# Performance work log

Hardware: AMD Instinct MI355X
Metric: run time of the kernel (lower is better)

The kernel has to match this reference:

```python
import jax, jax.numpy as jnp
import numpy as np

B, NQ, NKV, D = 2, 2048, 4096, 1024
H, DH = 16, 64            # qk_channels = v_channels = 1024 -> 16 heads x 64
HID = 2 * int(4.0 * D)    # GEGLU produces 8192 -> split into 2x4096
EPS = 1e-6


def layernorm(x, scale, bias):
    mu = jnp.mean(x, axis=-1, keepdims=True)
    var = jnp.mean(jnp.square(x - mu), axis=-1, keepdims=True)
    return (x - mu) * jax.lax.rsqrt(var + EPS) * scale + bias


def setup_inputs() -> dict:
    key = jax.random.key(0)
    ks = jax.random.split(key, 12)
    s = 0.02
    return {
        "inputs_q": jax.random.normal(ks[0], (B, NQ, D), jnp.float32),
        "inputs_kv": jax.random.normal(ks[1], (B, NKV, D), jnp.float32),
        "ln_q_scale": jnp.ones((D,), jnp.float32),
        "ln_q_bias": jnp.zeros((D,), jnp.float32),
        "ln_kv_scale": jnp.ones((D,), jnp.float32),
        "ln_kv_bias": jnp.zeros((D,), jnp.float32),
        "Wq": s * jax.random.normal(ks[2], (D, H, DH), jnp.float32),
        "bq": jnp.zeros((H, DH), jnp.float32),
        "Wk": s * jax.random.normal(ks[3], (D, H, DH), jnp.float32),
        "bk": jnp.zeros((H, DH), jnp.float32),
        "Wv": s * jax.random.normal(ks[4], (D, H, DH), jnp.float32),
        "bv": jnp.zeros((H, DH), jnp.float32),
        "Wo": s * jax.random.normal(ks[5], (H, DH, D), jnp.float32),
        "bo": jnp.zeros((D,), jnp.float32),
        "ln2_scale": jnp.ones((D,), jnp.float32),
        "ln2_bias": jnp.zeros((D,), jnp.float32),
        "W1": s * jax.random.normal(ks[6], (D, HID), jnp.float32),
        "b1": jnp.zeros((HID,), jnp.float32),
        "W2": s * jax.random.normal(ks[7], (HID // 2, D), jnp.float32),
        "b2": jnp.zeros((D,), jnp.float32),
    }


def reference(inputs_q, inputs_kv, ln_q_scale, ln_q_bias, ln_kv_scale, ln_kv_bias,
              Wq, bq, Wk, bk, Wv, bv, Wo, bo, ln2_scale, ln2_bias, W1, b1, W2, b2):
    ln_q = layernorm(inputs_q, ln_q_scale, ln_q_bias)
    ln_kv = layernorm(inputs_kv, ln_kv_scale, ln_kv_bias)
    # multi-head projections: DenseGeneral to (H, DH)
    q = jnp.einsum('bqd,dhe->bqhe', ln_q, Wq) + bq
    k = jnp.einsum('bkd,dhe->bkhe', ln_kv, Wk) + bk
    v = jnp.einsum('bkd,dhe->bkhe', ln_kv, Wv) + bv
    # scaled dot-product attention (full score matrix, as in source)
    attn = jnp.einsum('bqhd,bkhd->bhqk', q, k) / np.sqrt(DH).astype(np.float32)
    attn = jax.nn.softmax(attn, axis=-1)
    o = jnp.einsum('bhqk,bkhd->bqhd', attn, v)
    # output projection contracting (H, DH)
    x = jnp.einsum('bqhd,hdo->bqo', o, Wo) + bo
    x = x + inputs_q  # query residual
    # GEGLU MLP
    h = layernorm(x, ln2_scale, ln2_bias)
    h = jnp.dot(h, W1) + b1
    a, g = jnp.split(h, 2, axis=-1)
    h = a * jax.nn.gelu(g)  # approximate (tanh) gelu, flax default
    y = jnp.dot(h, W2) + b2
    return x + y
```

## Files before the change

kernel.cpp:

```cpp
#include <hip/hip_runtime.h>

typedef unsigned short u16;
typedef unsigned int u32;
typedef float f32x4 __attribute__((ext_vector_type(4)));
typedef float f32x16 __attribute__((ext_vector_type(16)));
typedef __bf16 bf16x8 __attribute__((ext_vector_type(8)));
typedef short s16x8 __attribute__((ext_vector_type(8)));
typedef short s16x4 __attribute__((ext_vector_type(4)));
typedef u32 u32x4 __attribute__((ext_vector_type(4)));

#define MFMA16(a, b, c) __builtin_amdgcn_mfma_f32_16x16x32_bf16((a), (b), (c), 0, 0, 0)
#define MFMA32(a, b, c) __builtin_amdgcn_mfma_f32_32x32x16_bf16((a), (b), (c), 0, 0, 0)

typedef const __attribute__((address_space(1))) void* gas1_t;
typedef __attribute__((address_space(3))) void* las3_t;
#define GLDS16(g, l) __builtin_amdgcn_global_load_lds((gas1_t)(g), (las3_t)(l), 16, 0, 0)

static __device__ __forceinline__ u16 f2bf(float f) {
  u32 u = __builtin_bit_cast(u32, f);
  u += 0x7FFFu + ((u >> 16) & 1u);
  return (u16)(u >> 16);
}
static __device__ __forceinline__ float bf2f(u16 h) {
  return __builtin_bit_cast(float, (u32)h << 16);
}
static __device__ __forceinline__ u32 cvtpk(float lo, float hi) {
  u32 r;
  asm("v_cvt_pk_bf16_f32 %0, %1, %2" : "=v"(r) : "v"(lo), "v"(hi));
  return r;
}

__global__ __launch_bounds__(256) void transp_cvt(const float* __restrict__ in,
                                                  u16* __restrict__ out, int K, int N,
                                                  float scale) {
  __shared__ u16 t[64][72];
  int k0 = blockIdx.x * 64, n0 = blockIdx.y * 64;
#pragma unroll
  for (int i = 0; i < 16; ++i) {
    int idx = threadIdx.x + i * 256;
    int r = idx >> 6, c = idx & 63;
    t[r][c] = f2bf(in[(size_t)(k0 + r) * N + n0 + c] * scale);
  }
  __syncthreads();
#pragma unroll
  for (int i = 0; i < 16; ++i) {
    int idx = threadIdx.x + i * 256;
    int r = idx >> 6, c = idx & 63;
    out[(size_t)(n0 + r) * K + k0 + c] = t[c][r];
  }
}

__global__ __launch_bounds__(256) void ln_bf16(const float* __restrict__ x,
                                               const float* __restrict__ sc,
                                               const float* __restrict__ bi,
                                               u16* __restrict__ out) {
  int row = blockIdx.x;
  int tid = threadIdx.x;
  float4 v = ((const float4*)(x + (size_t)row * 1024))[tid];
  float s = v.x + v.y + v.z + v.w;
  float s2 = v.x * v.x + v.y * v.y + v.z * v.z + v.w * v.w;
  for (int m = 1; m < 64; m <<= 1) {
    s += __shfl_xor(s, m);
    s2 += __shfl_xor(s2, m);
  }
  __shared__ float rs[4], rs2[4];
  int wave = tid >> 6, lane = tid & 63;
  if (lane == 0) { rs[wave] = s; rs2[wave] = s2; }
  __syncthreads();
  s = rs[0] + rs[1] + rs[2] + rs[3];
  s2 = rs2[0] + rs2[1] + rs2[2] + rs2[3];
  float mu = s * (1.0f / 1024.0f);
  float var = s2 * (1.0f / 1024.0f) - mu * mu;
  float inv = rsqrtf(var + 1e-6f);
  float4 scv = ((const float4*)sc)[tid];
  float4 biv = ((const float4*)bi)[tid];
  s16x4 o;
  o[0] = (short)f2bf((v.x - mu) * inv * scv.x + biv.x);
  o[1] = (short)f2bf((v.y - mu) * inv * scv.y + biv.y);
  o[2] = (short)f2bf((v.z - mu) * inv * scv.z + biv.z);
  o[3] = (short)f2bf((v.w - mu) * inv * scv.w + biv.w);
  *(s16x4*)(out + (size_t)row * 1024 + tid * 4) = o;
}

template <int MODE>
__global__ __launch_bounds__(256) void gemm_nt(const u16* __restrict__ A,
                                               const u16* __restrict__ Bt,
                                               const float* __restrict__ bias,
                                               const float* __restrict__ resid,
                                               void* __restrict__ Cout,
                                               int M, int N, int K, float bias_scale) {
  __shared__ u16 As[128 * 64];
  __shared__ u16 Bs[128 * 64];
  const int m0 = blockIdx.x * 128, n0 = blockIdx.y * 128;
  const int tid = threadIdx.x;
  const int lane = tid & 63, wave = tid >> 6;
  const int wm = (wave >> 1) * 64, wn = (wave & 1) * 64;
  const int lr = lane & 15, hi4 = lane >> 4;
  f32x4 acc[4][4] = {};
  for (int k0 = 0; k0 < K; k0 += 64) {
#pragma unroll
    for (int i = 0; i < 4; ++i) {
      int s = i * 256 + tid;
      int r = s >> 3, slot = s & 7;
      int gslot = slot ^ (r & 7);
      int ldst = (i * 256 + wave * 64) * 8;
      GLDS16(A + (size_t)(m0 + r) * K + k0 + gslot * 8, &As[ldst]);
      GLDS16(Bt + (size_t)(n0 + r) * K + k0 + gslot * 8, &Bs[ldst]);
    }
    __syncthreads();
#pragma unroll
    for (int ks = 0; ks < 2; ++ks) {
      const int sl = ((ks * 4 + hi4) ^ (lr & 7)) * 8;
      bf16x8 af[4], bfr[4];
#pragma unroll
      for (int t = 0; t < 4; ++t) {
        af[t] = __builtin_bit_cast(bf16x8, *(const s16x8*)&As[(wm + t * 16 + lr) * 64 + sl]);
        bfr[t] = __builtin_bit_cast(bf16x8, *(const s16x8*)&Bs[(wn + t * 16 + lr) * 64 + sl]);
      }
#pragma unroll
      for (int mt = 0; mt < 4; ++mt)
#pragma unroll
        for (int nt = 0; nt < 4; ++nt)
          acc[mt][nt] = MFMA16(af[mt], bfr[nt], acc[mt][nt]);
    }
    __syncthreads();
  }
#pragma unroll
  for (int mt = 0; mt < 4; ++mt) {
#pragma unroll
    for (int nt = 0; nt < 4; ++nt) {
      const int ncol = n0 + wn + nt * 16 + lr;
      const float bv = bias[ncol] * bias_scale;
      const int mbase = m0 + wm + mt * 16 + hi4 * 4;
#pragma unroll
      for (int r = 0; r < 4; ++r) {
        const int m = mbase + r;
        const float val = acc[mt][nt][r] + bv;
        if constexpr (MODE == 0) {
          ((u16*)Cout)[(size_t)m * N + ncol] = f2bf(val);
        } else if constexpr (MODE == 1) {
          size_t vidx = ((size_t)((m >> 12) * 1024 + ncol) << 12) | (size_t)(m & 4095);
          ((u16*)Cout)[vidx] = f2bf(val);
        } else {
          ((float*)Cout)[(size_t)m * N + ncol] = val + resid[(size_t)m * N + ncol];
        }
      }
    }
  }
}

__global__ __launch_bounds__(256, 2) void flash_attn(const u16* __restrict__ Qg,
                                                     const u16* __restrict__ Kg,
                                                     const u16* __restrict__ Vt,
                                                     u16* __restrict__ Og) {
  __shared__ u16 Ks[2][64 * 64];
  __shared__ u16 Vs[2][64 * 64];
  const int id = blockIdx.x;
  const int bh = (id & 7) * 4 + ((id >> 3) & 3);
  const int qb = id >> 5;
  const int b = bh >> 4, h = bh & 15;
  const int q0 = qb * 128;
  const int tid = threadIdx.x;
  const int lane = tid & 63, wave = tid >> 6;
  const int lq = lane & 31, hi = lane >> 5;
  const u16* Kbase = Kg + (size_t)(b * 4096) * 1024 + h * 64;
  const u16* Vbase = Vt + (size_t)((b * 16 + h) * 64) * 4096;
  bf16x8 qf[4];
  const size_t qrow = (size_t)(b * 2048 + q0 + wave * 32 + lq);
#pragma unroll
  for (int dc = 0; dc < 4; ++dc)
    qf[dc] = __builtin_bit_cast(bf16x8, *(const s16x8*)&Qg[qrow * 1024 + h * 64 + dc * 16 + hi * 8]);

  f32x16 oacc0 = {}, oacc1 = {};
  float lrun = 0.0f;

  auto stage = [&](int buf, int tile) {
    const int kv0 = tile * 64;
#pragma unroll
    for (int i = 0; i < 2; ++i) {
      int s = i * 256 + tid;
      int r = s >> 3;
      int inb = ((s & 7) * 16) ^ ((r & 7) << 4);
      GLDS16(Kbase + (size_t)(kv0 + r) * 1024 + (inb >> 1), &Ks[buf][(i * 256 + wave * 64) * 8]);
    }
#pragma unroll
    for (int i = 0; i < 2; ++i) {
      int s = i * 256 + tid;
      int r = s >> 3;
      int inb = ((s & 7) * 16) ^ ((r & 7) << 4);
      GLDS16(Vbase + (size_t)r * 4096 + kv0 + (inb >> 1), &Vs[buf][(i * 256 + wave * 64) * 8]);
    }
  };

  stage(0, 0);
  __syncthreads();
  int cur = 0;
  for (int t = 0; t < 64; ++t) {
    if (t < 63) stage(cur ^ 1, t + 1);
    f32x16 sA = {}, sB = {};
#pragma unroll
    for (int dc = 0; dc < 4; ++dc) {
      int row = lq;
      int inb = (dc * 32 + hi * 16) ^ ((row & 7) << 4);
      bf16x8 kf = __builtin_bit_cast(bf16x8, *(const s16x8*)&Ks[cur][row * 64 + (inb >> 1)]);
      sA = MFMA32(kf, qf[dc], sA);
    }
#pragma unroll
    for (int dc = 0; dc < 4; ++dc) {
      int row = 32 + lq;
      int inb = (dc * 32 + hi * 16) ^ ((row & 7) << 4);
      bf16x8 kf = __builtin_bit_cast(bf16x8, *(const s16x8*)&Ks[cur][row * 64 + (inb >> 1)]);
      sB = MFMA32(kf, qf[dc], sB);
    }
    float ts = 0.0f;
#pragma unroll
    for (int i = 0; i < 16; ++i) {
      float p = __builtin_amdgcn_exp2f(sA[i]);
      sA[i] = p;
      ts += p;
    }
#pragma unroll
    for (int i = 0; i < 16; ++i) {
      float p = __builtin_amdgcn_exp2f(sB[i]);
      sB[i] = p;
      ts += p;
    }
    ts += __shfl_xor(ts, 32);
    lrun += ts;
    u32 wa[8], wb[8];
#pragma unroll
    for (int i = 0; i < 8; ++i) wa[i] = cvtpk(sA[2 * i], sA[2 * i + 1]);
#pragma unroll
    for (int i = 0; i < 8; ++i) wb[i] = cvtpk(sB[2 * i], sB[2 * i + 1]);
    u32 a0 = wa[0], c0 = wa[2];
    asm("v_permlane32_swap_b32 %0, %1" : "+v"(a0), "+v"(c0));
    u32 a1 = wa[1], c1 = wa[3];
    asm("v_permlane32_swap_b32 %0, %1" : "+v"(a1), "+v"(c1));
    u32 a2 = wa[4], c2 = wa[6];
    asm("v_permlane32_swap_b32 %0, %1" : "+v"(a2), "+v"(c2));
    u32 a3 = wa[5], c3 = wa[7];
    asm("v_permlane32_swap_b32 %0, %1" : "+v"(a3), "+v"(c3));
    u32 e0 = wb[0], g0 = wb[2];
    asm("v_permlane32_swap_b32 %0, %1" : "+v"(e0), "+v"(g0));
    u32 e1 = wb[1], g1 = wb[3];
    asm("v_permlane32_swap_b32 %0, %1" : "+v"(e1), "+v"(g1));
    u32 e2 = wb[4], g2 = wb[6];
    asm("v_permlane32_swap_b32 %0, %1" : "+v"(e2), "+v"(g2));
    u32 e3 = wb[5], g3 = wb[7];
    asm("v_permlane32_swap_b32 %0, %1" : "+v"(e3), "+v"(g3));
    u32x4 t00 = {a0, a1, c0, c1};
    u32x4 t01 = {a2, a3, c2, c3};
    u32x4 t10 = {e0, e1, g0, g1};
    u32x4 t11 = {e2, e3, g2, g3};
    bf16x8 p00 = __builtin_bit_cast(bf16x8, t00);
    bf16x8 p01 = __builtin_bit_cast(bf16x8, t01);
    bf16x8 p10 = __builtin_bit_cast(bf16x8, t10);
    bf16x8 p11 = __builtin_bit_cast(bf16x8, t11);
#pragma unroll
    for (int st = 0; st < 2; ++st) {
      bf16x8 pc0 = st ? p10 : p00;
      bf16x8 pc1 = st ? p11 : p01;
#pragma unroll
      for (int c = 0; c < 2; ++c) {
        bf16x8 pf = c ? pc1 : pc0;
        {
          int row = lq;
          int inb = (st * 64 + c * 32 + hi * 16) ^ ((row & 7) << 4);
          bf16x8 vf = __builtin_bit_cast(bf16x8, *(const s16x8*)&Vs[cur][row * 64 + (inb >> 1)]);
          oacc0 = MFMA32(vf, pf, oacc0);
        }
        {
          int row = 32 + lq;
          int inb = (st * 64 + c * 32 + hi * 16) ^ ((row & 7) << 4);
          bf16x8 vf = __builtin_bit_cast(bf16x8, *(const s16x8*)&Vs[cur][row * 64 + (inb >> 1)]);
          oacc1 = MFMA32(vf, pf, oacc1);
        }
      }
    }
    __syncthreads();
    cur ^= 1;
  }
  float rinv = 1.0f / lrun;
  u16* obase = Og + qrow * 1024 + h * 64;
#pragma unroll
  for (int rp = 0; rp < 8; ++rp) {
    int r0 = rp * 2;
    int d0 = (r0 & 3) + 8 * (r0 >> 2) + 4 * hi;
    *(u32*)&obase[d0] = cvtpk(oacc0[r0] * rinv, oacc0[r0 + 1] * rinv);
    *(u32*)&obase[32 + d0] = cvtpk(oacc1[r0] * rinv, oacc1[r0 + 1] * rinv);
  }
}

__global__ __launch_bounds__(256) void geglu_k(const u16* __restrict__ h,
                                               u16* __restrict__ out) {
  size_t v = (size_t)blockIdx.x * 256 + threadIdx.x;
  size_t row = v >> 9, c8 = (v & 511) * 8;
  const u16* pa = h + row * 8192 + c8;
  s16x8 va = *(const s16x8*)pa;
  s16x8 vg = *(const s16x8*)(pa + 4096);
  s16x8 o;
#pragma unroll
  for (int j = 0; j < 8; ++j) {
    float a = bf2f((u16)va[j]);
    float gv = bf2f((u16)vg[j]);
    float u = 0.7978845608f * (gv + 0.044715f * gv * gv * gv);
    float e = __expf(2.0f * u);
    float t = 1.0f - 2.0f / (e + 1.0f);
    o[j] = (short)f2bf(a * 0.5f * gv * (1.0f + t));
  }
  *(s16x8*)(out + row * 4096 + c8) = o;
}

extern "C" void kernel_launch(void* const* d_in, const int* in_sizes, int n_in,
                              void* d_out, int out_size, void* d_ws, size_t ws_size,
                              hipStream_t stream) {
  (void)in_sizes; (void)n_in; (void)out_size; (void)ws_size;
  const float* inputs_q = (const float*)d_in[0];
  const float* inputs_kv = (const float*)d_in[1];
  const float* ln_q_scale = (const float*)d_in[2];
  const float* ln_q_bias = (const float*)d_in[3];
  const float* ln_kv_scale = (const float*)d_in[4];
  const float* ln_kv_bias = (const float*)d_in[5];
  const float* Wq = (const float*)d_in[6];
  const float* bq = (const float*)d_in[7];
  const float* Wk = (const float*)d_in[8];
  const float* bk = (const float*)d_in[9];
  const float* Wv = (const float*)d_in[10];
  const float* bv = (const float*)d_in[11];
  const float* Wo = (const float*)d_in[12];
  const float* bo = (const float*)d_in[13];
  const float* ln2_scale = (const float*)d_in[14];
  const float* ln2_bias = (const float*)d_in[15];
  const float* W1 = (const float*)d_in[16];
  const float* b1 = (const float*)d_in[17];
  const float* W2 = (const float*)d_in[18];
  const float* b2 = (const float*)d_in[19];
  float* out = (float*)d_out;
  char* ws = (char*)d_ws;
  const size_t MB = 1ull << 20;
  u16* lnq = (u16*)(ws + 0);
  u16* lnkv = (u16*)(ws + 8 * MB);
  u16* Qb = (u16*)(ws + 24 * MB);
  u16* Kb = (u16*)(ws + 32 * MB);
  u16* Vtb = (u16*)(ws + 48 * MB);
  u16* hfull = (u16*)(ws + 0);
  u16* Ob = (u16*)(ws + 64 * MB);
  float* xbuf = (float*)(ws + 72 * MB);
  u16* ln2b = (u16*)(ws + 88 * MB);
  u16* gg = (u16*)(ws + 96 * MB);
  u16* wqt = (u16*)(ws + 128 * MB);
  u16* wkt = (u16*)(ws + 130 * MB);
  u16* wvt = (u16*)(ws + 132 * MB);
  u16* wot = (u16*)(ws + 134 * MB);
  u16* w1t = (u16*)(ws + 136 * MB);
  u16* w2t = (u16*)(ws + 152 * MB);

  const float QSC = 0.125f * 1.44269504088896f;
  dim3 blk(256);
  transp_cvt<<<dim3(16, 16), blk, 0, stream>>>(Wq, wqt, 1024, 1024, QSC);
  transp_cvt<<<dim3(16, 16), blk, 0, stream>>>(Wk, wkt, 1024, 1024, 1.0f);
  transp_cvt<<<dim3(16, 16), blk, 0, stream>>>(Wv, wvt, 1024, 1024, 1.0f);
  transp_cvt<<<dim3(16, 16), blk, 0, stream>>>(Wo, wot, 1024, 1024, 1.0f);
  transp_cvt<<<dim3(16, 128), blk, 0, stream>>>(W1, w1t, 1024, 8192, 1.0f);
  transp_cvt<<<dim3(64, 16), blk, 0, stream>>>(W2, w2t, 4096, 1024, 1.0f);
  ln_bf16<<<4096, blk, 0, stream>>>(inputs_q, ln_q_scale, ln_q_bias, lnq);
  ln_bf16<<<8192, blk, 0, stream>>>(inputs_kv, ln_kv_scale, ln_kv_bias, lnkv);
  gemm_nt<0><<<dim3(32, 8), blk, 0, stream>>>(lnq, wqt, bq, nullptr, Qb, 4096, 1024, 1024, QSC);
  gemm_nt<0><<<dim3(64, 8), blk, 0, stream>>>(lnkv, wkt, bk, nullptr, Kb, 8192, 1024, 1024, 1.0f);
  gemm_nt<1><<<dim3(64, 8), blk, 0, stream>>>(lnkv, wvt, bv, nullptr, Vtb, 8192, 1024, 1024, 1.0f);
  flash_attn<<<dim3(512), blk, 0, stream>>>(Qb, Kb, Vtb, Ob);
  gemm_nt<2><<<dim3(32, 8), blk, 0, stream>>>(Ob, wot, bo, inputs_q, xbuf, 4096, 1024, 1024, 1.0f);
  ln_bf16<<<4096, blk, 0, stream>>>(xbuf, ln2_scale, ln2_bias, ln2b);
  gemm_nt<0><<<dim3(32, 64), blk, 0, stream>>>(ln2b, w1t, b1, nullptr, hfull, 4096, 8192, 1024, 1.0f);
  geglu_k<<<8192, blk, 0, stream>>>(hfull, gg);
  gemm_nt<2><<<dim3(32, 8), blk, 0, stream>>>(gg, w2t, b2, xbuf, out, 4096, 1024, 4096, 1.0f);
}
```

Before: 409.8 us.

## Add 256x256 GEMM, fuse K/V projections and GEGLU into W1 GEMM

Adds a new 512-thread gemm256 kernel with 256x256 tiles, a 4-stage LDS pipeline using global_load_lds, and s_setprio around the MFMA blocks. The K and V projections are merged into one GEMM over concatenated weights, with the epilogue splitting the output into K and transposed V. W1 columns are interleaved so each wave holds matching a/gate columns, which lets the GEGLU run in the GEMM epilogue and removes the 8192-wide intermediate round trip and the separate geglu kernel. Flash attention also gets setprio hints around its MFMA sections. The larger tiles and LDS use may limit occupancy.

```diff
diff --git a/kernel.cpp b/kernel.cpp
--- a/kernel.cpp
+++ b/kernel.cpp
@@ -29,6 +29,12 @@
   asm("v_cvt_pk_bf16_f32 %0, %1, %2" : "=v"(r) : "v"(lo), "v"(hi));
   return r;
 }
+static __device__ __forceinline__ float gelu_t(float g) {
+  float u = 0.7978845608f * (g + 0.044715f * g * g * g);
+  float e = __expf(2.0f * u);
+  float t = 1.0f - 2.0f / (e + 1.0f);
+  return 0.5f * g * (1.0f + t);
+}
 
 __global__ __launch_bounds__(256) void transp_cvt(const float* __restrict__ in,
                                                   u16* __restrict__ out, int K, int N,
@@ -47,6 +53,27 @@
     int idx = threadIdx.x + i * 256;
     int r = idx >> 6, c = idx & 63;
     out[(size_t)(n0 + r) * K + k0 + c] = t[c][r];
+  }
+}
+
+__global__ __launch_bounds__(256) void geglu_transp(const float* __restrict__ in,
+                                                    u16* __restrict__ out) {
+  __shared__ u16 t[64][72];
+  int k0 = blockIdx.x * 64, n0 = blockIdx.y * 64;
+#pragma unroll
+  for (int i = 0; i < 16; ++i) {
+    int idx = threadIdx.x + i * 256;
+    int r = idx >> 6, c = idx & 63;
+    int np = n0 + c;
+    int orig = ((np >> 5) << 4) + (np & 15) + (((np >> 4) & 1) << 12);
+    t[r][c] = f2bf(in[(size_t)(k0 + r) * 8192 + orig]);
+  }
+  __syncthreads();
+#pragma unroll
+  for (int i = 0; i < 16; ++i) {
+    int idx = threadIdx.x + i * 256;
+    int r = idx >> 6, c = idx & 63;
+    out[(size_t)(n0 + r) * 1024 + k0 + c] = t[c][r];
   }
 }
 
@@ -143,6 +170,140 @@
           ((u16*)Cout)[vidx] = f2bf(val);
         } else {
           ((float*)Cout)[(size_t)m * N + ncol] = val + resid[(size_t)m * N + ncol];
+        }
+      }
+    }
+  }
+}
+
+template <int MODE>
+__global__ __launch_bounds__(512, 2) void gemm256(const u16* __restrict__ A,
+                                                  const u16* __restrict__ Bt,
+                                                  const float* __restrict__ bias,
+                                                  const float* __restrict__ bias2,
+                                                  u16* __restrict__ Cout,
+                                                  u16* __restrict__ Vout,
+                                                  int M, int N, int K) {
+  __shared__ u16 lds[4][2][8192];
+  const int nbx = M >> 8;
+  const int nblk = nbx * (N >> 8);
+  const int cpx = nblk >> 3;
+  const int wg0 = blockIdx.x;
+  const int wg = (wg0 & 7) * cpx + (wg0 >> 3);
+  const int m0 = (wg % nbx) * 256, n0 = (wg / nbx) * 256;
+  const int tid = threadIdx.x;
+  const int lane = tid & 63, wave = tid >> 6;
+  const int wr = wave >> 2, wc = wave & 3;
+  const int lr = lane & 15, hi4 = lane >> 4;
+  const int rslot = (hi4 ^ ((lr >> 1) & 3)) * 8;
+  const int NT = K >> 5;
+
+  auto stageA = [&](int u) {
+    const int buf = u & 3;
+#pragma unroll
+    for (int i = 0; i < 2; ++i) {
+      int s = i * 512 + tid;
+      int r = s >> 2, slot = s & 3;
+      int gs = slot ^ ((r >> 1) & 3);
+      GLDS16(A + (size_t)(m0 + r) * K + u * 32 + gs * 8,
+             &lds[buf][0][(i * 512 + wave * 64) * 8]);
+    }
+  };
+  auto stageB = [&](int u) {
+    const int buf = u & 3;
+#pragma unroll
+    for (int i = 0; i < 2; ++i) {
+      int s = i * 512 + tid;
+      int r = s >> 2, slot = s & 3;
+      int gs = slot ^ ((r >> 1) & 3);
+      GLDS16(Bt + (size_t)(n0 + r) * K + u * 32 + gs * 8,
+             &lds[buf][1][(i * 512 + wave * 64) * 8]);
+    }
+  };
+
+  f32x4 acc[8][4] = {};
+  stageA(0); stageB(0); stageA(1); stageB(1); stageA(2); stageB(2);
+  asm volatile("s_waitcnt vmcnt(8)" ::: "memory");
+  __builtin_amdgcn_s_barrier();
+
+  for (int t = 0; t < NT; ++t) {
+    const int buf = t & 3;
+    const u16* Ab = lds[buf][0];
+    const u16* Bb = lds[buf][1];
+    bf16x8 bfr[4], af[4];
+#pragma unroll
+    for (int nt = 0; nt < 4; ++nt)
+      bfr[nt] = __builtin_bit_cast(bf16x8, *(const s16x8*)&Bb[(wc * 64 + nt * 16 + lr) * 32 + rslot]);
+#pragma unroll
+    for (int mt = 0; mt < 4; ++mt)
+      af[mt] = __builtin_bit_cast(bf16x8, *(const s16x8*)&Ab[(wr * 128 + mt * 16 + lr) * 32 + rslot]);
+    if (t + 3 < NT) stageA(t + 3);
+    __builtin_amdgcn_s_setprio(1);
+#pragma unroll
+    for (int mt = 0; mt < 4; ++mt)
+#pragma unroll
+      for (int nt = 0; nt < 4; ++nt)
+        acc[mt][nt] = MFMA16(af[mt], bfr[nt], acc[mt][nt]);
+    __builtin_amdgcn_s_setprio(0);
+#pragma unroll
+    for (int mt = 0; mt < 4; ++mt)
+      af[mt] = __builtin_bit_cast(bf16x8, *(const s16x8*)&Ab[(wr * 128 + 64 + mt * 16 + lr) * 32 + rslot]);
+    if (t + 3 < NT) stageB(t + 3);
+    __builtin_amdgcn_s_setprio(1);
+#pragma unroll
+    for (int mt = 0; mt < 4; ++mt)
+#pragma unroll
+      for (int nt = 0; nt < 4; ++nt)
+        acc[4 + mt][nt] = MFMA16(af[mt], bfr[nt], acc[4 + mt][nt]);
+    __builtin_amdgcn_s_setprio(0);
+    if (t + 3 < NT)
+      asm volatile("s_waitcnt vmcnt(8)" ::: "memory");
+    else if (t + 2 < NT)
+      asm volatile("s_waitcnt vmcnt(4)" ::: "memory");
+    else
+      asm volatile("s_waitcnt vmcnt(0)" ::: "memory");
+    __builtin_amdgcn_s_barrier();
+  }
+
+  if constexpr (MODE == 0) {
+#pragma unroll
+    for (int mf = 0; mf < 8; ++mf) {
+#pragma unroll
+      for (int nt = 0; nt < 4; ++nt) {
+        const int ncol = n0 + wc * 64 + nt * 16 + lr;
+        const int mbase = m0 + wr * 128 + mf * 16 + hi4 * 4;
+        const bool isk = ncol < 1024;
+        const int vc = isk ? ncol : ncol - 1024;
+        const float bv = isk ? bias[ncol] : bias2[vc];
+#pragma unroll
+        for (int r = 0; r < 4; ++r) {
+          const int m = mbase + r;
+          const float val = acc[mf][nt][r] + bv;
+          if (isk) {
+            Cout[(size_t)m * 1024 + ncol] = f2bf(val);
+          } else {
+            size_t vidx = ((size_t)((m >> 12) * 1024 + vc) << 12) | (size_t)(m & 4095);
+            Vout[vidx] = f2bf(val);
+          }
+        }
+      }
+    }
+  } else {
+#pragma unroll
+    for (int mf = 0; mf < 8; ++mf) {
+      const int mbase = m0 + wr * 128 + mf * 16 + hi4 * 4;
+#pragma unroll
+      for (int p = 0; p < 2; ++p) {
+        const int acol = n0 + wc * 64 + p * 32 + lr;
+        const int oc = ((acol >> 5) << 4) + lr;
+        const float ba = bias[oc];
+        const float bg = bias[oc + 4096];
+#pragma unroll
+        for (int r = 0; r < 4; ++r) {
+          const int m = mbase + r;
+          float a = acc[mf][2 * p][r] + ba;
+          float g = acc[mf][2 * p + 1][r] + bg;
+          Cout[(size_t)m * 4096 + oc] = f2bf(a * gelu_t(g));
         }
       }
     }
@@ -198,6 +359,7 @@
   for (int t = 0; t < 64; ++t) {
     if (t < 63) stage(cur ^ 1, t + 1);
     f32x16 sA = {}, sB = {};
+    __builtin_amdgcn_s_setprio(1);
 #pragma unroll
     for (int dc = 0; dc < 4; ++dc) {
       int row = lq;
@@ -212,6 +374,7 @@
       bf16x8 kf = __builtin_bit_cast(bf16x8, *(const s16x8*)&Ks[cur][row * 64 + (inb >> 1)]);
       sB = MFMA32(kf, qf[dc], sB);
     }
+    __builtin_amdgcn_s_setprio(0);
     float ts = 0.0f;
 #pragma unroll
     for (int i = 0; i < 16; ++i) {
@@ -256,6 +419,7 @@
     bf16x8 p01 = __builtin_bit_cast(bf16x8, t01);
     bf16x8 p10 = __builtin_bit_cast(bf16x8, t10);
     bf16x8 p11 = __builtin_bit_cast(bf16x8, t11);
+    __builtin_amdgcn_s_setprio(1);
 #pragma unroll
     for (int st = 0; st < 2; ++st) {
       bf16x8 pc0 = st ? p10 : p00;
@@ -277,6 +441,7 @@
         }
       }
     }
+    __builtin_amdgcn_s_setprio(0);
     __syncthreads();
     cur ^= 1;
   }
@@ -289,26 +454,6 @@
     *(u32*)&obase[d0] = cvtpk(oacc0[r0] * rinv, oacc0[r0 + 1] * rinv);
     *(u32*)&obase[32 + d0] = cvtpk(oacc1[r0] * rinv, oacc1[r0 + 1] * rinv);
   }
-}
-
-__global__ __launch_bounds__(256) void geglu_k(const u16* __restrict__ h,
-                                               u16* __restrict__ out) {
-  size_t v = (size_t)blockIdx.x * 256 + threadIdx.x;
-  size_t row = v >> 9, c8 = (v & 511) * 8;
-  const u16* pa = h + row * 8192 + c8;
-  s16x8 va = *(const s16x8*)pa;
-  s16x8 vg = *(const s16x8*)(pa + 4096);
-  s16x8 o;
-#pragma unroll
-  for (int j = 0; j < 8; ++j) {
-    float a = bf2f((u16)va[j]);
-    float gv = bf2f((u16)vg[j]);
-    float u = 0.7978845608f * (gv + 0.044715f * gv * gv * gv);
-    float e = __expf(2.0f * u);
-    float t = 1.0f - 2.0f / (e + 1.0f);
-    o[j] = (short)f2bf(a * 0.5f * gv * (1.0f + t));
-  }
-  *(s16x8*)(out + row * 4096 + c8) = o;
 }
 
 extern "C" void kernel_launch(void* const* d_in, const int* in_sizes, int n_in,
@@ -343,35 +488,31 @@
   u16* Qb = (u16*)(ws + 24 * MB);
   u16* Kb = (u16*)(ws + 32 * MB);
   u16* Vtb = (u16*)(ws + 48 * MB);
-  u16* hfull = (u16*)(ws + 0);
   u16* Ob = (u16*)(ws + 64 * MB);
   float* xbuf = (float*)(ws + 72 * MB);
   u16* ln2b = (u16*)(ws + 88 * MB);
   u16* gg = (u16*)(ws + 96 * MB);
   u16* wqt = (u16*)(ws + 128 * MB);
-  u16* wkt = (u16*)(ws + 130 * MB);
-  u16* wvt = (u16*)(ws + 132 * MB);
+  u16* wkvt = (u16*)(ws + 130 * MB);
   u16* wot = (u16*)(ws + 134 * MB);
-  u16* w1t = (u16*)(ws + 136 * MB);
+  u16* w1i = (u16*)(ws + 136 * MB);
   u16* w2t = (u16*)(ws + 152 * MB);
 
   const float QSC = 0.125f * 1.44269504088896f;
   dim3 blk(256);
   transp_cvt<<<dim3(16, 16), blk, 0, stream>>>(Wq, wqt, 1024, 1024, QSC);
-  transp_cvt<<<dim3(16, 16), blk, 0, stream>>>(Wk, wkt, 1024, 1024, 1.0f);
-  transp_cvt<<<dim3(16, 16), blk, 0, stream>>>(Wv, wvt, 1024, 1024, 1.0f);
+  transp_cvt<<<dim3(16, 16), blk, 0, stream>>>(Wk, wkvt, 1024, 1024, 1.0f);
+  transp_cvt<<<dim3(16, 16), blk, 0, stream>>>(Wv, wkvt + 1024 * 1024, 1024, 1024, 1.0f);
   transp_cvt<<<dim3(16, 16), blk, 0, stream>>>(Wo, wot, 1024, 1024, 1.0f);
-  transp_cvt<<<dim3(16, 128), blk, 0, stream>>>(W1, w1t, 1024, 8192, 1.0f);
+  geglu_transp<<<dim3(16, 128), blk, 0, stream>>>(W1, w1i);
   transp_cvt<<<dim3(64, 16), blk, 0, stream>>>(W2, w2t, 4096, 1024, 1.0f);
   ln_bf16<<<4096, blk, 0, stream>>>(inputs_q, ln_q_scale, ln_q_bias, lnq);
   ln_bf16<<<8192, blk, 0, stream>>>(inputs_kv, ln_kv_scale, ln_kv_bias, lnkv);
   gemm_nt<0><<<dim3(32, 8), blk, 0, stream>>>(lnq, wqt, bq, nullptr, Qb, 4096, 1024, 1024, QSC);
-  gemm_nt<0><<<dim3(64, 8), blk, 0, stream>>>(lnkv, wkt, bk, nullptr, Kb, 8192, 1024, 1024, 1.0f);
-  gemm_nt<1><<<dim3(64, 8), blk, 0, stream>>>(lnkv, wvt, bv, nullptr, Vtb, 8192, 1024, 1024, 1.0f);
+  gemm256<0><<<dim3(256), dim3(512), 0, stream>>>(lnkv, wkvt, bk, bv, Kb, Vtb, 8192, 2048, 1024);
   flash_attn<<<dim3(512), blk, 0, stream>>>(Qb, Kb, Vtb, Ob);
   gemm_nt<2><<<dim3(32, 8), blk, 0, stream>>>(Ob, wot, bo, inputs_q, xbuf, 4096, 1024, 1024, 1.0f);
   ln_bf16<<<4096, blk, 0, stream>>>(xbuf, ln2_scale, ln2_bias, ln2b);
-  gemm_nt<0><<<dim3(32, 64), blk, 0, stream>>>(ln2b, w1t, b1, nullptr, hfull, 4096, 8192, 1024, 1.0f);
-  geglu_k<<<8192, blk, 0, stream>>>(hfull, gg);
+  gemm256<1><<<dim3(512), dim3(512), 0, stream>>>(ln2b, w1i, b1, nullptr, gg, nullptr, 4096, 8192, 1024);
   gemm_nt<2><<<dim3(32, 8), blk, 0, stream>>>(gg, w2t, b2, xbuf, out, 4096, 1024, 4096, 1.0f);
 }
```

Result: no change. 411.6 us (+0.5%).
